# Performance work log

Hardware: AMD Instinct MI355X
Metric: run time of the kernel (lower is better)

## Reference

```python
import jax, jax.numpy as jnp
import numpy as np

N = 200000
E = 200000
H = 256
NEG_INF = -1e30


def setup_inputs() -> dict:
    key = jax.random.key(0)
    k1, k2, k3, k4, k5, k6, k7 = jax.random.split(key, 7)
    node_tokens = jax.random.normal(k1, (N, H), dtype=jnp.float32)
    relation_tokens = jax.random.normal(k2, (E, H), dtype=jnp.float32)
    edge_index = jax.random.randint(k3, (2, E), 0, N, dtype=jnp.int64)
    node_is_cvt = jax.random.randint(k4, (N,), 0, 2) > 0
    # learned params (randomized for a non-trivial test; torch inits attn/shared to zeros)
    shared_cvt = jax.random.normal(k5, (H,), dtype=jnp.float32) * 0.02
    attn_vector = jax.random.normal(k6, (H,), dtype=jnp.float32) * 0.1
    W_msg = jax.random.normal(k7, (H, 2 * H), dtype=jnp.float32) * (1.0 / np.sqrt(2 * H))  # torch Linear weight [out,in]
    return {"node_tokens": node_tokens, "relation_tokens": relation_tokens,
            "edge_index": edge_index, "node_is_cvt": node_is_cvt,
            "shared_cvt": shared_cvt, "attn_vector": attn_vector, "W_msg": W_msg}


def reference(node_tokens, relation_tokens, edge_index, node_is_cvt, shared_cvt, attn_vector, W_msg):
    num_nodes, hidden = node_tokens.shape
    num_edges = relation_tokens.shape[0]
    tails = edge_index[1]                      # [E]
    cvt_mask = node_is_cvt.astype(bool)        # [N]
    edge_mask = cvt_mask[tails]                # [E] edges whose tail is a CVT node

    # faithful quirk: nbr token for edge i is node_tokens[i] (edge slot index)
    nbr = node_tokens[:num_edges]                                   # [E, H]
    msg = jnp.concatenate([relation_tokens, nbr], axis=-1) @ W_msg.T  # [E, H]

    # per-edge logits, segment-wise (per tail node) softmax over CVT-tail edges only
    logits = jnp.where(edge_mask, jnp.einsum('eh,h->e', msg, attn_vector), NEG_INF)
    m = jax.ops.segment_max(logits, tails, num_segments=num_nodes)   # [N]
    p = jnp.where(edge_mask, jnp.exp(logits - m[tails]), 0.0)        # [E]
    denom = jax.ops.segment_sum(p, tails, num_segments=num_nodes)    # [N]
    w = p / jnp.where(denom > 0, denom, 1.0)[tails]                  # [E]

    agg = jax.ops.segment_sum(msg * w[:, None], tails, num_segments=num_nodes)  # [N, H]
    cvt_tokens = agg + shared_cvt
    return jnp.where(cvt_mask[:, None], cvt_tokens, node_tokens)
```

## Files before the change

### kernel.cpp

```cpp
#include <hip/hip_runtime.h>
#include <math.h>

#define H   256
#define H2  512
#define MX  16

typedef __attribute__((ext_vector_type(4))) float f32x4;
typedef __attribute__((ext_vector_type(8))) short short8;

__device__ __forceinline__ short f2bf(float f) {
  unsigned u = __builtin_bit_cast(unsigned, f);
  u = (u + 0x7FFFu + ((u >> 16) & 1u)) >> 16;
  return (short)u;
}

__device__ __forceinline__ void gload_lds16(const void* g, void* l) {
  __builtin_amdgcn_global_load_lds(
      (const __attribute__((address_space(1))) unsigned int*)g,
      (__attribute__((address_space(3))) unsigned int*)l, 16, 0, 0);
}

__global__ void k_init(unsigned* cnt, int* ctrs, int N) {
  int i = blockIdx.x * blockDim.x + threadIdx.x;
  if (i < N) cnt[i] = 0u;
  if (i == 0) { ctrs[0] = 0; }
}

__global__ void k_prep(const int* __restrict__ ei, const int* __restrict__ cvt,
                       const float* __restrict__ W, const float* __restrict__ attn,
                       unsigned* __restrict__ cnt, int* __restrict__ ebuf,
                       float* __restrict__ u, short* __restrict__ Wt, int E) {
  int g = blockIdx.x * blockDim.x + threadIdx.x;
  if (g < E) {
    int tail = ei[E + g];
    if (cvt[tail]) {
      unsigned pos = atomicAdd(cnt + tail, 1u);
      if (pos < MX) ebuf[(size_t)tail * MX + pos] = g;
    }
  }
  if (g < 512) {
    float s = 0.f;
    for (int h = 0; h < H; ++h) s += W[(size_t)h * H2 + g] * attn[h];
    u[g] = s;
  }
  if (g < 16384) {
    int n = g & 255, kb = g >> 8;
    const float* src = W + (size_t)n * H2 + kb * 8;
    f32x4 a = *(const f32x4*)src;
    f32x4 b = *(const f32x4*)(src + 4);
    short8 o;
    o[0]=f2bf(a.x); o[1]=f2bf(a.y); o[2]=f2bf(a.z); o[3]=f2bf(a.w);
    o[4]=f2bf(b.x); o[5]=f2bf(b.y); o[6]=f2bf(b.z); o[7]=f2bf(b.w);
    *(short8*)(Wt + (size_t)(kb * 256 + n) * 8) = o;
  }
}

__global__ void k_slots(const unsigned* __restrict__ cnt, int* __restrict__ ctrs,
                        int* __restrict__ actpk, int N) {
  int n = blockIdx.x * blockDim.x + threadIdx.x;
  int lane = threadIdx.x & 63;
  unsigned c = (n < N) ? cnt[n] : 0u;
  bool active = c > 0u;
  unsigned long long mask = __ballot(active);
  if (!mask) return;
  int rank = __popcll(mask & ((1ull << lane) - 1ull));
  int wcount = __popcll(mask);
  int sbase = 0;
  if (lane == 0) sbase = atomicAdd(ctrs + 0, wcount);
  sbase = __shfl(sbase, 0);
  if (active) {
    int cc = (int)(c > MX ? MX : c);
    actpk[sbase + rank] = n | (cc << 20);
  }
}

__global__ __launch_bounds__(256) void k_fin(
    const float* __restrict__ NT, const int* __restrict__ cvt,
    const unsigned* __restrict__ cnt, const float* __restrict__ sc,
    const float* __restrict__ R, const float* __restrict__ u,
    const int* __restrict__ actpk, const int* __restrict__ ctrs,
    const int* __restrict__ ebuf, short* __restrict__ Ast,
    float* __restrict__ out, int N) {
  int wid = blockIdx.x * 4 + (threadIdx.x >> 6);
  int nw = gridDim.x * 4;
  int lane = threadIdx.x & 63;

  auto outinit = [&]() {
    f32x4 scl = ((const f32x4*)sc)[lane];
    for (int row = wid; row < N; row += nw) {
      int cv = cvt[row];
      if (cv && cnt[row] > 0u) continue;
      f32x4 v = cv ? scl : ((const f32x4*)NT)[(size_t)row * 64 + lane];
      ((f32x4*)out)[(size_t)row * 64 + lane] = v;
    }
  };

  auto gather = [&]() {
    int nAct = ctrs[0];
    int loff = lane * 8;
    const float* src0 = (loff < H) ? (R + loff) : (NT + (loff - H));
    const f32x4* u4 = (const f32x4*)u;
    f32x4 ua = u4[lane * 2], ub = u4[lane * 2 + 1];
    int s = wid;
    if (s >= nAct) return;
    int pk = actpk[s];
    int n = pk & 0xFFFFF, c = pk >> 20;
    int id = (lane < c) ? ebuf[(size_t)n * MX + lane] : 0;
    while (true) {
      int s2 = s + nw;
      int n2 = 0, c2 = 0, id2 = 0;
      if (s2 < nAct) {
        int pk2 = actpk[s2];
        n2 = pk2 & 0xFFFFF; c2 = pk2 >> 20;
        id2 = (lane < c2) ? ebuf[(size_t)n2 * MX + lane] : 0;
      }
      f32x4 x0, x1;
      if (c == 1) {
        int e = __shfl(id, 0);
        const f32x4* src = (const f32x4*)(src0 + (size_t)e * H);
        x0 = src[0]; x1 = src[1];
      } else if (c == 2) {
        int e0 = __shfl(id, 0), e1 = __shfl(id, 1);
        const f32x4* sA = (const f32x4*)(src0 + (size_t)e0 * H);
        const f32x4* sB = (const f32x4*)(src0 + (size_t)e1 * H);
        f32x4 a0 = sA[0], b0 = sA[1], a1 = sB[0], b1 = sB[1];
        float d0 = a0.x*ua.x + a0.y*ua.y + a0.z*ua.z + a0.w*ua.w
                 + b0.x*ub.x + b0.y*ub.y + b0.z*ub.z + b0.w*ub.w;
        float d1 = a1.x*ua.x + a1.y*ua.y + a1.z*ua.z + a1.w*ua.w
                 + b1.x*ub.x + b1.y*ub.y + b1.z*ub.z + b1.w*ub.w;
        #pragma unroll
        for (int off = 32; off > 0; off >>= 1) {
          d0 += __shfl_xor(d0, off);
          d1 += __shfl_xor(d1, off);
        }
        float p0 = __expf(d0), p1 = __expf(d1);
        float inv = 1.f / (p0 + p1);
        p0 *= inv; p1 *= inv;
        x0 = a0 * p0 + a1 * p1;
        x1 = b0 * p0 + b1 * p1;
      } else {
        x0 = (f32x4){0.f,0.f,0.f,0.f}; x1 = x0;
        float den = 0.f;
        for (int i = 0; i < c; ++i) {
          int e = __shfl(id, i);
          const f32x4* src = (const f32x4*)(src0 + (size_t)e * H);
          f32x4 a = src[0], b = src[1];
          float d = a.x*ua.x + a.y*ua.y + a.z*ua.z + a.w*ua.w
                  + b.x*ub.x + b.y*ub.y + b.z*ub.z + b.w*ub.w;
          #pragma unroll
          for (int off = 32; off > 0; off >>= 1) d += __shfl_xor(d, off);
          float pe = __expf(d);
          den += pe;
          x0 += a * pe;
          x1 += b * pe;
        }
        float inv = 1.f / den;
        x0 *= inv; x1 *= inv;
      }
      short8 o;
      o[0]=f2bf(x0.x); o[1]=f2bf(x0.y); o[2]=f2bf(x0.z); o[3]=f2bf(x0.w);
      o[4]=f2bf(x1.x); o[5]=f2bf(x1.y); o[6]=f2bf(x1.z); o[7]=f2bf(x1.w);
      *(short8*)(Ast + (size_t)s * H2 + loff) = o;
      if (s2 >= nAct) break;
      s = s2; n = n2; c = c2; id = id2;
    }
  };

  if (wid & 1) { gather(); outinit(); }
  else         { outinit(); gather(); }
}

__global__ __launch_bounds__(256) void k_gemm2(
    const short* __restrict__ Wt, const short* __restrict__ Ast,
    const int* __restrict__ actpk, const int* __restrict__ ctrs,
    const float* __restrict__ sc, float* __restrict__ out) {
  __shared__ __align__(16) short Bs[2][4][256][8];
  __shared__ __align__(16) short As[2][4][128][8];
  int nAct = ctrs[0];
  int base = blockIdx.x * 128;
  if (base >= nAct) return;
  int tid = threadIdx.x;
  int wave = tid >> 6, lane = tid & 63;
  int l15 = lane & 15, lg = lane >> 4;

  int row0 = base + lane;       if (row0 >= nAct) row0 = nAct - 1;
  int row1 = base + 64 + lane;  if (row1 >= nAct) row1 = nAct - 1;
  const short* arow0 = Ast + (size_t)row0 * H2;
  const short* arow1 = Ast + (size_t)row1 * H2;

  auto stage = [&](int b, int kk) {
    gload_lds16(arow0 + kk + wave * 8, &As[b][wave][0][0]);
    gload_lds16(arow1 + kk + wave * 8, &As[b][wave][64][0]);
    int kb = kk >> 3;
    #pragma unroll
    for (int it = 0; it < 4; ++it) {
      const short* src = Wt + (size_t)(kb + it) * 2048 + (size_t)tid * 8;
      gload_lds16(src, &Bs[b][it][wave * 64][0]);
    }
  };

  f32x4 acc[8][4];
  #pragma unroll
  for (int i = 0; i < 8; ++i)
    #pragma unroll
    for (int j = 0; j < 4; ++j) acc[i][j] = (f32x4){0.f, 0.f, 0.f, 0.f};

  stage(0, 0);
  __syncthreads();
  int cur = 0;
  for (int t = 0; t < 16; ++t) {
    if (t < 15) stage(cur ^ 1, (t + 1) * 32);
    short8 bf[4];
    #pragma unroll
    for (int ct = 0; ct < 4; ++ct)
      bf[ct] = *(const short8*)&Bs[cur][lg][wave * 64 + ct * 16 + l15][0];
    #pragma unroll
    for (int rt = 0; rt < 8; ++rt) {
      short8 af = *(const short8*)&As[cur][lg][rt * 16 + l15][0];
      #pragma unroll
      for (int ct = 0; ct < 4; ++ct)
        acc[rt][ct] = __builtin_amdgcn_mfma_f32_16x16x32_bf16(af, bf[ct], acc[rt][ct], 0, 0, 0);
    }
    __syncthreads();
    cur ^= 1;
  }

  #pragma unroll
  for (int rt = 0; rt < 8; ++rt) {
    #pragma unroll
    for (int rr = 0; rr < 4; ++rr) {
      int sD = base + rt * 16 + lg * 4 + rr;
      if (sD >= nAct) continue;
      int n = actpk[sD] & 0xFFFFF;
      float* orow = out + (size_t)n * H;
      #pragma unroll
      for (int ct = 0; ct < 4; ++ct) {
        int c = wave * 64 + ct * 16 + l15;
        __builtin_nontemporal_store(acc[rt][ct][rr] + sc[c], orow + c);
      }
    }
  }
}

extern "C" void kernel_launch(void* const* d_in, const int* in_sizes, int n_in,
                              void* d_out, int out_size, void* d_ws, size_t ws_size,
                              hipStream_t stream) {
  const float* NT   = (const float*)d_in[0];
  const float* R    = (const float*)d_in[1];
  const int*   ei   = (const int*)d_in[2];
  const int*   cvt  = (const int*)d_in[3];
  const float* sc   = (const float*)d_in[4];
  const float* attn = (const float*)d_in[5];
  const float* W    = (const float*)d_in[6];
  float* out = (float*)d_out;

  int N = in_sizes[0] / H;
  int E = in_sizes[1] / H;

  char* wsp = (char*)d_ws;
  auto alloc = [&](size_t bytes) { char* r = wsp; wsp += (bytes + 255) & ~(size_t)255; return r; };
  float*    u       = (float*)alloc(512 * 4);
  short*    Wt      = (short*)alloc((size_t)H * H2 * 2);
  int*      ebuf    = (int*)alloc((size_t)N * MX * 4);
  short*    Ast     = (short*)alloc((size_t)N * H2 * 2);
  unsigned* cnt     = (unsigned*)alloc((size_t)N * 4);
  int*      actpk   = (int*)alloc((size_t)N * 4);
  int*      ctrs    = (int*)alloc(2 * 4);

  k_init<<<(N + 255) / 256, 256, 0, stream>>>(cnt, ctrs, N);
  k_prep<<<(E + 255) / 256, 256, 0, stream>>>(ei, cvt, W, attn, cnt, ebuf, u, Wt, E);
  k_slots<<<(N + 255) / 256, 256, 0, stream>>>(cnt, ctrs, actpk, N);
  k_fin<<<2048, 256, 0, stream>>>(NT, cvt, cnt, sc, R, u, actpk, ctrs, ebuf, Ast, out, N);
  k_gemm2<<<(N + 127) / 128, 256, 0, stream>>>(Wt, Ast, actpk, ctrs, sc, out);
}
```

Measured before the change: 212.3 us.

## Batch row metadata loads per wave and pair gathers for more loads in flight

The output-init loop now loads cvt/cnt flags for 8 rows at once per wave and broadcasts them with shuffles, instead of issuing scalar loads row by row. The gather loop processes active slots in chunks of 8. It prefetches pack words and the first two edge ids per lane, then issues the row loads for two slots before computing either, to raise memory-level parallelism. The init kernel is replaced with hipMemsetAsync calls. This adds shuffle overhead and register pressure, and slots with more than two edges still take a serial path.

New measurement: 220.3 us. +3.8%, slower.

```diff
diff --git a/kernel.cpp b/kernel.cpp
--- a/kernel.cpp
+++ b/kernel.cpp
@@ -18,12 +18,6 @@
   __builtin_amdgcn_global_load_lds(
       (const __attribute__((address_space(1))) unsigned int*)g,
       (__attribute__((address_space(3))) unsigned int*)l, 16, 0, 0);
-}
-
-__global__ void k_init(unsigned* cnt, int* ctrs, int N) {
-  int i = blockIdx.x * blockDim.x + threadIdx.x;
-  if (i < N) cnt[i] = 0u;
-  if (i == 0) { ctrs[0] = 0; }
 }
 
 __global__ void k_prep(const int* __restrict__ ei, const int* __restrict__ cvt,
@@ -87,11 +81,17 @@
 
   auto outinit = [&]() {
     f32x4 scl = ((const f32x4*)sc)[lane];
-    for (int row = wid; row < N; row += nw) {
-      int cv = cvt[row];
-      if (cv && cnt[row] > 0u) continue;
-      f32x4 v = cv ? scl : ((const f32x4*)NT)[(size_t)row * 64 + lane];
-      ((f32x4*)out)[(size_t)row * 64 + lane] = v;
+    for (int cb = wid * 8; cb < N; cb += nw * 8) {
+      int nr = N - cb; if (nr > 8) nr = 8;
+      int cvl = (lane < nr) ? cvt[cb + lane] : 1;
+      unsigned ctl = (lane < nr) ? cnt[cb + lane] : 1u;
+      for (int j = 0; j < nr; ++j) {
+        int cv = __shfl(cvl, j);
+        unsigned ct = __shfl(ctl, j);
+        if (cv && ct > 0u) continue;
+        f32x4 v = cv ? scl : ((const f32x4*)NT)[(size_t)(cb + j) * 64 + lane];
+        ((f32x4*)out)[(size_t)(cb + j) * 64 + lane] = v;
+      }
     }
   };
 
@@ -101,33 +101,17 @@
     const float* src0 = (loff < H) ? (R + loff) : (NT + (loff - H));
     const f32x4* u4 = (const f32x4*)u;
     f32x4 ua = u4[lane * 2], ub = u4[lane * 2 + 1];
-    int s = wid;
-    if (s >= nAct) return;
-    int pk = actpk[s];
-    int n = pk & 0xFFFFF, c = pk >> 20;
-    int id = (lane < c) ? ebuf[(size_t)n * MX + lane] : 0;
-    while (true) {
-      int s2 = s + nw;
-      int n2 = 0, c2 = 0, id2 = 0;
-      if (s2 < nAct) {
-        int pk2 = actpk[s2];
-        n2 = pk2 & 0xFFFFF; c2 = pk2 >> 20;
-        id2 = (lane < c2) ? ebuf[(size_t)n2 * MX + lane] : 0;
-      }
+
+    auto procStore = [&](int slot, int n_, int c_,
+                         f32x4 r0, f32x4 r1, f32x4 r2, f32x4 r3) {
       f32x4 x0, x1;
-      if (c == 1) {
-        int e = __shfl(id, 0);
-        const f32x4* src = (const f32x4*)(src0 + (size_t)e * H);
-        x0 = src[0]; x1 = src[1];
-      } else if (c == 2) {
-        int e0 = __shfl(id, 0), e1 = __shfl(id, 1);
-        const f32x4* sA = (const f32x4*)(src0 + (size_t)e0 * H);
-        const f32x4* sB = (const f32x4*)(src0 + (size_t)e1 * H);
-        f32x4 a0 = sA[0], b0 = sA[1], a1 = sB[0], b1 = sB[1];
-        float d0 = a0.x*ua.x + a0.y*ua.y + a0.z*ua.z + a0.w*ua.w
-                 + b0.x*ub.x + b0.y*ub.y + b0.z*ub.z + b0.w*ub.w;
-        float d1 = a1.x*ua.x + a1.y*ua.y + a1.z*ua.z + a1.w*ua.w
-                 + b1.x*ub.x + b1.y*ub.y + b1.z*ub.z + b1.w*ub.w;
+      if (c_ == 1) {
+        x0 = r0; x1 = r1;
+      } else if (c_ == 2) {
+        float d0 = r0.x*ua.x + r0.y*ua.y + r0.z*ua.z + r0.w*ua.w
+                 + r1.x*ub.x + r1.y*ub.y + r1.z*ub.z + r1.w*ub.w;
+        float d1 = r2.x*ua.x + r2.y*ua.y + r2.z*ua.z + r2.w*ua.w
+                 + r3.x*ub.x + r3.y*ub.y + r3.z*ub.z + r3.w*ub.w;
         #pragma unroll
         for (int off = 32; off > 0; off >>= 1) {
           d0 += __shfl_xor(d0, off);
@@ -136,13 +120,14 @@
         float p0 = __expf(d0), p1 = __expf(d1);
         float inv = 1.f / (p0 + p1);
         p0 *= inv; p1 *= inv;
-        x0 = a0 * p0 + a1 * p1;
-        x1 = b0 * p0 + b1 * p1;
+        x0 = r0 * p0 + r2 * p1;
+        x1 = r1 * p0 + r3 * p1;
       } else {
+        int idg = (lane < c_) ? ebuf[(size_t)n_ * MX + lane] : 0;
         x0 = (f32x4){0.f,0.f,0.f,0.f}; x1 = x0;
         float den = 0.f;
-        for (int i = 0; i < c; ++i) {
-          int e = __shfl(id, i);
+        for (int i = 0; i < c_; ++i) {
+          int e = __shfl(idg, i);
           const f32x4* src = (const f32x4*)(src0 + (size_t)e * H);
           f32x4 a = src[0], b = src[1];
           float d = a.x*ua.x + a.y*ua.y + a.z*ua.z + a.w*ua.w
@@ -160,9 +145,37 @@
       short8 o;
       o[0]=f2bf(x0.x); o[1]=f2bf(x0.y); o[2]=f2bf(x0.z); o[3]=f2bf(x0.w);
       o[4]=f2bf(x1.x); o[5]=f2bf(x1.y); o[6]=f2bf(x1.z); o[7]=f2bf(x1.w);
-      *(short8*)(Ast + (size_t)s * H2 + loff) = o;
-      if (s2 >= nAct) break;
-      s = s2; n = n2; c = c2; id = id2;
+      *(short8*)(Ast + (size_t)slot * H2 + loff) = o;
+    };
+
+    for (int cb = wid * 8; cb < nAct; cb += nw * 8) {
+      int nc = nAct - cb; if (nc > 8) nc = 8;
+      int myPk = (lane < nc) ? actpk[cb + lane] : 0;
+      int myN = myPk & 0xFFFFF, myC = myPk >> 20;
+      int myI0 = 0, myI1 = 0;
+      if (lane < nc && myC >= 1) myI0 = ebuf[(size_t)myN * MX];
+      if (lane < nc && myC >= 2) myI1 = ebuf[(size_t)myN * MX + 1];
+      for (int j = 0; j < nc; j += 2) {
+        int pkA = __shfl(myPk, j);
+        int nA = pkA & 0xFFFFF, cA = pkA >> 20;
+        int a0 = __shfl(myI0, j), a1 = __shfl(myI1, j);
+        int pkB = (j + 1 < nc) ? __shfl(myPk, j + 1) : 0;
+        int nB = pkB & 0xFFFFF, cB = pkB >> 20;
+        int b0 = __shfl(myI0, j + 1), b1 = __shfl(myI1, j + 1);
+        f32x4 A0, A1, A2, A3, B0, B1, B2, B3;
+        if (cA >= 1 && cA <= 2) {
+          const f32x4* s = (const f32x4*)(src0 + (size_t)a0 * H);
+          A0 = s[0]; A1 = s[1];
+          if (cA == 2) { const f32x4* t = (const f32x4*)(src0 + (size_t)a1 * H); A2 = t[0]; A3 = t[1]; }
+        }
+        if (cB >= 1 && cB <= 2) {
+          const f32x4* s = (const f32x4*)(src0 + (size_t)b0 * H);
+          B0 = s[0]; B1 = s[1];
+          if (cB == 2) { const f32x4* t = (const f32x4*)(src0 + (size_t)b1 * H); B2 = t[0]; B3 = t[1]; }
+        }
+        procStore(cb + j, nA, cA, A0, A1, A2, A3);
+        if (cB >= 1) procStore(cb + j + 1, nB, cB, B0, B1, B2, B3);
+      }
     }
   };
 
@@ -267,7 +280,8 @@
   int*      actpk   = (int*)alloc((size_t)N * 4);
   int*      ctrs    = (int*)alloc(2 * 4);
 
-  k_init<<<(N + 255) / 256, 256, 0, stream>>>(cnt, ctrs, N);
+  hipMemsetAsync(cnt, 0, (size_t)N * 4, stream);
+  hipMemsetAsync(ctrs, 0, 8, stream);
   k_prep<<<(E + 255) / 256, 256, 0, stream>>>(ei, cvt, W, attn, cnt, ebuf, u, Wt, E);
   k_slots<<<(N + 255) / 256, 256, 0, stream>>>(cnt, ctrs, actpk, N);
   k_fin<<<2048, 256, 0, stream>>>(NT, cvt, cnt, sc, R, u, actpk, ctrs, ebuf, Ast, out, N);
```

## Route single-edge CVT nodes to a direct GEMM, skipping the gather staging

Applied to the files above, without the earlier changes.

Nodes with exactly one incoming CVT edge get softmax weight 1, so their message is just W applied to the fp32 relation/node rows. `k_slots` now compacts these nodes into a separate list. A new `k_gemmD` kernel streams their fp32 rows straight into LDS, converts them to bf16 on the fly and runs MFMA, writing the output directly. This avoids the bf16 Ast write and re-read for the most common active case. The zeroing kernel is replaced by hipMemsetAsync. The cost is an extra kernel launch, a second atomic-compacted list, and a dependence on k_fin's output init not overwriting those rows.

Measured after the change: 284.4 us. 33.9% more time.

```diff
diff --git a/kernel.cpp b/kernel.cpp
--- a/kernel.cpp
+++ b/kernel.cpp
@@ -18,12 +18,6 @@
   __builtin_amdgcn_global_load_lds(
       (const __attribute__((address_space(1))) unsigned int*)g,
       (__attribute__((address_space(3))) unsigned int*)l, 16, 0, 0);
-}
-
-__global__ void k_init(unsigned* cnt, int* ctrs, int N) {
-  int i = blockIdx.x * blockDim.x + threadIdx.x;
-  if (i < N) cnt[i] = 0u;
-  if (i == 0) { ctrs[0] = 0; }
 }
 
 __global__ void k_prep(const int* __restrict__ ei, const int* __restrict__ cvt,
@@ -55,22 +49,114 @@
   }
 }
 
-__global__ void k_slots(const unsigned* __restrict__ cnt, int* __restrict__ ctrs,
-                        int* __restrict__ actpk, int N) {
+__global__ void k_slots(const unsigned* __restrict__ cnt, const int* __restrict__ ebuf,
+                        int* __restrict__ ctrs, int* __restrict__ actpk,
+                        int* __restrict__ actc1, int* __restrict__ eid1c, int N) {
   int n = blockIdx.x * blockDim.x + threadIdx.x;
   int lane = threadIdx.x & 63;
   unsigned c = (n < N) ? cnt[n] : 0u;
-  bool active = c > 0u;
-  unsigned long long mask = __ballot(active);
-  if (!mask) return;
-  int rank = __popcll(mask & ((1ull << lane) - 1ull));
-  int wcount = __popcll(mask);
-  int sbase = 0;
-  if (lane == 0) sbase = atomicAdd(ctrs + 0, wcount);
-  sbase = __shfl(sbase, 0);
-  if (active) {
-    int cc = (int)(c > MX ? MX : c);
-    actpk[sbase + rank] = n | (cc << 20);
+  bool is2 = c >= 2u, is1 = c == 1u;
+  unsigned long long m2 = __ballot(is2);
+  if (m2) {
+    int rank = __popcll(m2 & ((1ull << lane) - 1ull));
+    int wc = __popcll(m2);
+    int base = 0;
+    if (lane == 0) base = atomicAdd(ctrs + 0, wc);
+    base = __shfl(base, 0);
+    if (is2) {
+      int cc = (int)(c > MX ? MX : c);
+      actpk[base + rank] = n | (cc << 20);
+    }
+  }
+  unsigned long long m1 = __ballot(is1);
+  if (m1) {
+    int rank = __popcll(m1 & ((1ull << lane) - 1ull));
+    int wc = __popcll(m1);
+    int base = 0;
+    if (lane == 0) base = atomicAdd(ctrs + 1, wc);
+    base = __shfl(base, 0);
+    if (is1) {
+      actc1[base + rank] = n;
+      eid1c[base + rank] = ebuf[(size_t)n * MX];
+    }
+  }
+}
+
+__global__ __launch_bounds__(256) void k_gemmD(
+    const float* __restrict__ R, const float* __restrict__ NT,
+    const short* __restrict__ Wt, const int* __restrict__ actc1,
+    const int* __restrict__ eid1c, const int* __restrict__ ctrs,
+    const float* __restrict__ sc, float* __restrict__ out) {
+  __shared__ __align__(16) float Asf[2][4][2][64][4];
+  __shared__ __align__(16) short Bs[2][4][256][8];
+  int nc1 = ctrs[1];
+  int base = blockIdx.x * 64;
+  if (base >= nc1) return;
+  int tid = threadIdx.x, wave = tid >> 6, lane = tid & 63;
+  int l15 = lane & 15, lg = lane >> 4;
+
+  int r = base + lane; if (r >= nc1) r = nc1 - 1;
+  int e = eid1c[r];
+  const float* p0 = R + (size_t)e * H;
+  const float* p1 = NT + (size_t)e * H;
+
+  auto stage = [&](int b, int kk) {
+    const float* ph = (kk < H) ? p0 : p1;
+    int ko = kk & (H - 1);
+    gload_lds16(ph + ko + wave * 8,     &Asf[b][wave][0][0][0]);
+    gload_lds16(ph + ko + wave * 8 + 4, &Asf[b][wave][1][0][0]);
+    int kb = kk >> 3;
+    #pragma unroll
+    for (int it = 0; it < 4; ++it)
+      gload_lds16(Wt + (size_t)(kb + it) * 2048 + (size_t)tid * 8,
+                  &Bs[b][it][wave * 64][0]);
+  };
+
+  f32x4 acc[4][4];
+  #pragma unroll
+  for (int i = 0; i < 4; ++i)
+    #pragma unroll
+    for (int j = 0; j < 4; ++j) acc[i][j] = (f32x4){0.f, 0.f, 0.f, 0.f};
+
+  stage(0, 0);
+  __syncthreads();
+  int cur = 0;
+  for (int t = 0; t < 16; ++t) {
+    if (t < 15) stage(cur ^ 1, (t + 1) * 32);
+    short8 bf[4];
+    #pragma unroll
+    for (int ct = 0; ct < 4; ++ct)
+      bf[ct] = *(const short8*)&Bs[cur][lg][wave * 64 + ct * 16 + l15][0];
+    #pragma unroll
+    for (int rt = 0; rt < 4; ++rt) {
+      int row = rt * 16 + l15;
+      f32x4 fa = *(const f32x4*)&Asf[cur][lg][0][row][0];
+      f32x4 fb = *(const f32x4*)&Asf[cur][lg][1][row][0];
+      short8 af;
+      af[0]=f2bf(fa.x); af[1]=f2bf(fa.y); af[2]=f2bf(fa.z); af[3]=f2bf(fa.w);
+      af[4]=f2bf(fb.x); af[5]=f2bf(fb.y); af[6]=f2bf(fb.z); af[7]=f2bf(fb.w);
+      #pragma unroll
+      for (int ct = 0; ct < 4; ++ct)
+        acc[rt][ct] = __builtin_amdgcn_mfma_f32_16x16x32_bf16(af, bf[ct], acc[rt][ct], 0, 0, 0);
+    }
+    __syncthreads();
+    cur ^= 1;
+  }
+
+  #pragma unroll
+  for (int rt = 0; rt < 4; ++rt) {
+    #pragma unroll
+    for (int rr = 0; rr < 4; ++rr) {
+      int sD = base + rt * 16 + lg * 4 + rr;
+      if (sD >= nc1) continue;
+      int n = actc1[sD];
+      float* orow = out + (size_t)n * H;
+      #pragma unroll
+      for (int ct = 0; ct < 4; ++ct) {
+        int c = wave * 64 + ct * 16 + l15;
+        __builtin_nontemporal_store(acc[rt][ct][rr] + sc[c], orow + c);
+      }
+    }
   }
 }
 
@@ -115,11 +201,7 @@
         id2 = (lane < c2) ? ebuf[(size_t)n2 * MX + lane] : 0;
       }
       f32x4 x0, x1;
-      if (c == 1) {
-        int e = __shfl(id, 0);
-        const f32x4* src = (const f32x4*)(src0 + (size_t)e * H);
-        x0 = src[0]; x1 = src[1];
-      } else if (c == 2) {
+      if (c == 2) {
         int e0 = __shfl(id, 0), e1 = __shfl(id, 1);
         const f32x4* sA = (const f32x4*)(src0 + (size_t)e0 * H);
         const f32x4* sB = (const f32x4*)(src0 + (size_t)e1 * H);
@@ -170,7 +252,7 @@
   else         { outinit(); gather(); }
 }
 
-__global__ __launch_bounds__(256) void k_gemm2(
+__global__ __launch_bounds__(256) void k_gemmS(
     const short* __restrict__ Wt, const short* __restrict__ Ast,
     const int* __restrict__ actpk, const int* __restrict__ ctrs,
     const float* __restrict__ sc, float* __restrict__ out) {
@@ -265,11 +347,15 @@
   short*    Ast     = (short*)alloc((size_t)N * H2 * 2);
   unsigned* cnt     = (unsigned*)alloc((size_t)N * 4);
   int*      actpk   = (int*)alloc((size_t)N * 4);
+  int*      actc1   = (int*)alloc((size_t)N * 4);
+  int*      eid1c   = (int*)alloc((size_t)N * 4);
   int*      ctrs    = (int*)alloc(2 * 4);
 
-  k_init<<<(N + 255) / 256, 256, 0, stream>>>(cnt, ctrs, N);
+  hipMemsetAsync(cnt, 0, (size_t)N * 4, stream);
+  hipMemsetAsync(ctrs, 0, 8, stream);
   k_prep<<<(E + 255) / 256, 256, 0, stream>>>(ei, cvt, W, attn, cnt, ebuf, u, Wt, E);
-  k_slots<<<(N + 255) / 256, 256, 0, stream>>>(cnt, ctrs, actpk, N);
+  k_slots<<<(N + 255) / 256, 256, 0, stream>>>(cnt, ebuf, ctrs, actpk, actc1, eid1c, N);
+  k_gemmD<<<(N + 63) / 64, 256, 0, stream>>>(R, NT, Wt, actc1, eid1c, ctrs, sc, out);
   k_fin<<<2048, 256, 0, stream>>>(NT, cvt, cnt, sc, R, u, actpk, ctrs, ebuf, Ast, out, N);
-  k_gemm2<<<(N + 127) / 128, 256, 0, stream>>>(Wt, Ast, actpk, ctrs, sc, out);
-}
+  k_gemmS<<<(N + 127) / 128, 256, 0, stream>>>(Wt, Ast, actpk, ctrs, sc, out);
+}
```
